# Kernel tuning notes

Hardware: AMD Instinct MI355X
Metric: run time of the kernel (lower is better)

## Reference

```python
import jax, jax.numpy as jnp
import numpy as np

SOS = 28          # RNNTParam.SOS = num_labels - 1
NUM_EMBED = 28    # num_labels - 1
C = 320           # pred_hidden_size
L = 2             # pred_num_layers
U, N = 128, 512   # decode steps, batch


def setup_inputs() -> dict:
    key = jax.random.key(0)
    ks = jax.random.split(key, 8)
    s = 1.0 / np.sqrt(C).astype(np.float32)
    x = jax.random.randint(ks[0], (U, N), 0, 29)                       # labels incl. SOS=28
    h0 = jax.random.normal(ks[1], (L, N, C), jnp.float32)
    c0 = jax.random.normal(ks[2], (L, N, C), jnp.float32)
    embed_weight = jax.random.normal(ks[3], (NUM_EMBED, C), jnp.float32)
    w_ih = jax.random.uniform(ks[4], (L, 4 * C, C), jnp.float32, -s, s)
    w_hh = jax.random.uniform(ks[5], (L, 4 * C, C), jnp.float32, -s, s)
    b_ih = jax.random.uniform(ks[6], (L, 4 * C), jnp.float32, -s, s)
    b_hh = jax.random.uniform(ks[7], (L, 4 * C), jnp.float32, -s, s)
    return dict(x=x, h0=h0, c0=c0, embed_weight=embed_weight,
                w_ih=w_ih, w_hh=w_hh, b_ih=b_ih, b_hh=b_hh)


def _lstm_layer(xs, h0, c0, w_ih, w_hh, b_ih, b_hh):
    # xs: [U, N, C]; torch LSTM gate order: i, f, g, o
    bias = b_ih + b_hh                                   # [4C]
    gx = jnp.einsum('unc,gc->ung', xs, w_ih) + bias      # precompute input part

    def step(carry, gx_t):
        h, c = carry
        gates = gx_t + h @ w_hh.T                        # [N, 4C]
        i, f, g, o = jnp.split(gates, 4, axis=-1)
        i = jax.nn.sigmoid(i)
        f = jax.nn.sigmoid(f)
        g = jnp.tanh(g)
        o = jax.nn.sigmoid(o)
        c = f * c + i * g
        h = o * jnp.tanh(c)
        return (h, c), h

    (hT, cT), ys = jax.lax.scan(step, (h0, c0), gx)
    return ys, hT, cT


def reference(x, h0, c0, embed_weight, w_ih, w_hh, b_ih, b_hh):
    sos_mask = (x == SOS)                                # [U, N]
    idx = jnp.where(sos_mask, 0, x)
    g = embed_weight[idx]                                # [U, N, C]
    g = jnp.where(sos_mask[..., None], 0.0, g)

    hs, cs = [], []
    for layer in range(L):
        g, hT, cT = _lstm_layer(g, h0[layer], c0[layer],
                                w_ih[layer], w_hh[layer],
                                b_ih[layer], b_hh[layer])
        hs.append(hT)
        cs.append(cT)
    hg = jnp.stack(hs, axis=0)                           # [L, N, C]
    cg = jnp.stack(cs, axis=0)
    return g, (hg, cg)
```

## Files before the change

kernel.cpp:

```cpp
#include <hip/hip_runtime.h>
#include <hip/hip_bf16.h>
#include <stdint.h>


typedef short short8 __attribute__((ext_vector_type(8)));
typedef float f32x4 __attribute__((ext_vector_type(4)));

#define USTEPS 128
#define HSZ    (512*320)
#define GSTEP  (512*320)
#define HGOFF  (128*512*320)
#define CGOFF  (HGOFF + 2*512*320)
#define FLAGSTRIDE 16

__device__ __forceinline__ uint16_t f2bf(float f) {
  union { float f; uint32_t i; } v; v.f = f;
  uint32_t i = v.i;
  return (uint16_t)((i + 0x7fffu + ((i >> 16) & 1u)) >> 16);
}
__device__ __forceinline__ float rcp_(float x) { return __builtin_amdgcn_rcpf(x); }
__device__ __forceinline__ float sigm(float x) { return rcp_(1.0f + __expf(-x)); }
__device__ __forceinline__ float tanh_(float x) {
  float ax = fabsf(x);
  float e  = __expf(-2.0f * ax);
  float t  = (1.0f - e) * rcp_(1.0f + e);
  return x < 0.0f ? -t : t;
}
__device__ __forceinline__ uint4 cvt8(const float* s) {
  float4 a = ((const float4*)s)[0];
  float4 b = ((const float4*)s)[1];
  uint4 r;
  r.x = (uint32_t)f2bf(a.x) | ((uint32_t)f2bf(a.y) << 16);
  r.y = (uint32_t)f2bf(a.z) | ((uint32_t)f2bf(a.w) << 16);
  r.z = (uint32_t)f2bf(b.x) | ((uint32_t)f2bf(b.y) << 16);
  r.w = (uint32_t)f2bf(b.z) | ((uint32_t)f2bf(b.w) << 16);
  return r;
}
__device__ __forceinline__ short8 loadw8(const float* p) {
  float4 a = ((const float4*)p)[0];
  float4 b = ((const float4*)p)[1];
  short8 r;
  r[0] = (short)f2bf(a.x); r[1] = (short)f2bf(a.y);
  r[2] = (short)f2bf(a.z); r[3] = (short)f2bf(a.w);
  r[4] = (short)f2bf(b.x); r[5] = (short)f2bf(b.y);
  r[6] = (short)f2bf(b.z); r[7] = (short)f2bf(b.w);
  return r;
}

#define PREP_G0   (29 * 1280)
#define PREP_B1   (PREP_G0 + 1280)
#define PREP_FL   (PREP_B1 + 8192)
#define PREP_HI   (PREP_FL + 2 * 512 * 40)
__global__ void prep_kernel(const float* __restrict__ embed,
                            const float* __restrict__ w_ih,
                            const float* __restrict__ b_ih,
                            const float* __restrict__ b_hh,
                            const float* __restrict__ h0,
                            float* __restrict__ G0p,
                            float* __restrict__ bias1p,
                            uint32_t* __restrict__ flags,
                            uint16_t* __restrict__ Hx0,
                            uint16_t* __restrict__ Hx1) {
  int tid = blockIdx.x * blockDim.x + threadIdx.x;
  if (tid < PREP_G0) {
    int v = tid / 1280, col = tid % 1280;
    int hg = col / 80, idx = col % 80;
    int k = idx >> 2, q = idx & 3;
    int r = q * 320 + hg * 20 + k;
    float acc = b_ih[r] + b_hh[r];
    if (v < 28) {
      const float4* e = (const float4*)(embed + (size_t)v * 320);
      const float4* w = (const float4*)(w_ih + (size_t)r * 320);
#pragma unroll 4
      for (int i = 0; i < 80; ++i) {
        float4 a = e[i], b = w[i];
        acc += a.x * b.x + a.y * b.y + a.z * b.z + a.w * b.w;
      }
    }
    G0p[tid] = acc;
  } else if (tid < PREP_B1) {
    int col = tid - PREP_G0;
    int hg = col / 80, idx = col % 80;
    int k = idx >> 2, q = idx & 3;
    int r = q * 320 + hg * 20 + k;
    bias1p[col] = b_ih[1280 + r] + b_hh[1280 + r];
  } else if (tid < PREP_FL) {
    flags[tid - PREP_B1] = 0;
  } else if (tid < PREP_HI) {
    int id = tid - PREP_FL;
    int layer = id / 20480;
    int rem = id - layer * 20480;
    int n = rem / 40, c = rem - n * 40;
    const float* src = h0 + (size_t)layer * HSZ + (size_t)n * 320 + c * 8;
    uint16_t* dst = (layer ? Hx1 : Hx0) + HSZ + (size_t)n * 320 + c * 8;
    *(uint4*)dst = cvt8(src);
  }
}

__global__ void __launch_bounds__(320, 2)
rnnt_kernel(const int* __restrict__ x,
            const float* __restrict__ c0,
            const float* __restrict__ w_ih,
            const float* __restrict__ w_hh,
            const float* __restrict__ G0p,
            const float* __restrict__ bias1p,
            uint16_t* __restrict__ Hx0,
            uint16_t* __restrict__ Hx1,
            uint32_t* __restrict__ flags,
            float* __restrict__ out) {
  __shared__ __align__(16) uint16_t Hl0[32 * 320];
  __shared__ __align__(16) uint16_t Hl1[32 * 320];
  __shared__ __align__(16) float    gates0[32 * 84];
  __shared__ __align__(16) float    gates1[32 * 84];
  __shared__ int ctr0, ctr1;

  const int tid  = threadIdx.x;
  const int wave = tid >> 6;
  const int lane = tid & 63;
  const int quad = lane >> 4;
  const int lm   = lane & 15;
  const int blk  = blockIdx.x;
  const int bg = (blk & 7) * 2 + (blk >> 7);
  const int hg = (blk >> 3) & 15;

  short8 Bhh0[10], Bih1[10], Bhh1[10];
  {
    int ncol = wave * 16 + lm;
    int k = ncol >> 2, q = ncol & 3;
    int r = q * 320 + hg * 20 + k;
    const float* p0 = w_hh + (size_t)r * 320 + quad * 8;
    const float* p1 = w_hh + (size_t)(1280 + r) * 320 + quad * 8;
    const float* pi = w_ih + (size_t)(1280 + r) * 320 + quad * 8;
#pragma unroll
    for (int kk = 0; kk < 10; ++kk) {
      Bhh0[kk] = loadw8(p0 + kk * 32);
      Bhh1[kk] = loadw8(p1 + kk * 32);
      Bih1[kk] = loadw8(pi + kk * 32);
    }
  }
  const float bias1v = bias1p[hg * 80 + wave * 16 + lm];

  const int un  = tid / 10;
  const int ukp = tid - un * 10;
  const int n_g = bg * 32 + un;
  const int kc  = hg * 20 + ukp * 2;

  int smc[8], spc[8];
#pragma unroll
  for (int it = 0; it < 8; ++it) {
    int cid = tid + it * 320;
    int m = cid / 80;
    int c8 = cid - m * 80;
    int c16 = c8 >> 1, h = c8 & 1;
    int p16 = c16 + m; if (p16 >= 40) p16 -= 40;
    smc[it] = m * 320 + c8 * 4;
    spc[it] = m * 320 + p16 * 8 + h * 4;
  }
  const size_t gbase = (size_t)bg * 32 * 320;

  float c0s0 = c0[(size_t)n_g * 320 + kc];
  float c0s1 = c0[(size_t)n_g * 320 + kc + 1];
  float c1s0 = c0[(size_t)(512 + n_g) * 320 + kc];
  float c1s1 = c0[(size_t)(512 + n_g) * 320 + kc + 1];

  uint32_t* flags0  = flags;
  uint32_t* flags1  = flags + 256 * FLAGSTRIDE;
  uint32_t* myflag0 = flags0 + (size_t)(bg * 16 + hg) * FLAGSTRIDE;
  uint32_t* myflag1 = flags1 + (size_t)(bg * 16 + hg) * FLAGSTRIDE;

  {
    if (tid == 0) { ctr0 = 0; ctr1 = 0; }
    const uint16_t* s0b = Hx0 + HSZ + gbase;
    unsigned long long r0[8];
#pragma unroll
    for (int it = 0; it < 8; ++it)
      r0[it] = __hip_atomic_load((const unsigned long long*)(s0b + smc[it]),
                                 __ATOMIC_RELAXED, __HIP_MEMORY_SCOPE_AGENT);
    asm volatile("s_waitcnt vmcnt(0)" ::: "memory");
#pragma unroll
    for (int it = 0; it < 8; ++it)
      *(unsigned long long*)(Hl0 + spc[it]) = r0[it];
    __syncthreads();
  }

  float4 gxa, gxb;
  {
    const int v = x[n_g];
    const float* gx = G0p + (size_t)v * 1280 + hg * 80 + ukp * 8;
    gxa = ((const float4*)gx)[0];
    gxb = ((const float4*)gx)[1];
  }

#pragma unroll 1
  for (int t = 0; t <= USTEPS; ++t) {
    const bool do0 = (t < USTEPS);
    const bool do1 = (t >= 1);

    unsigned long long r1[8];
    if (do1) {
      const uint16_t* s1b = Hx1 + (size_t)(t & 1) * HSZ + gbase;
#pragma unroll
      for (int it = 0; it < 8; ++it)
        r1[it] = __hip_atomic_load((const unsigned long long*)(s1b + smc[it]),
                                   __ATOMIC_RELAXED, __HIP_MEMORY_SCOPE_AGENT);
    }

    f32x4 ag00 = {0.f, 0.f, 0.f, 0.f}, ag01 = {0.f, 0.f, 0.f, 0.f};
    f32x4 ag10 = {bias1v, bias1v, bias1v, bias1v}, ag11 = ag10;
#pragma unroll
    for (int kk = 0; kk < 10; ++kk) {
      int cch = kk * 4 + quad;
      int p0a = cch + lm;      if (p0a >= 40) p0a -= 40;
      int p1a = cch + lm + 16; if (p1a >= 40) p1a -= 40;
      short8 a00 = *(const short8*)(Hl0 + lm * 320 + p0a * 8);
      short8 a01 = *(const short8*)(Hl0 + (lm + 16) * 320 + p1a * 8);
      if (do0) {
        ag00 = __builtin_amdgcn_mfma_f32_16x16x32_bf16(a00, Bhh0[kk], ag00, 0, 0, 0);
        ag01 = __builtin_amdgcn_mfma_f32_16x16x32_bf16(a01, Bhh0[kk], ag01, 0, 0, 0);
      }
      if (do1) {
        ag10 = __builtin_amdgcn_mfma_f32_16x16x32_bf16(a00, Bih1[kk], ag10, 0, 0, 0);
        ag11 = __builtin_amdgcn_mfma_f32_16x16x32_bf16(a01, Bih1[kk], ag11, 0, 0, 0);
      }
    }

    if (do1) {
      asm volatile("s_waitcnt vmcnt(0)" ::: "memory");
#pragma unroll
      for (int it = 0; it < 8; ++it)
        *(unsigned long long*)(Hl1 + spc[it]) = r1[it];
    }
    if (do0) {
#pragma unroll
      for (int r = 0; r < 4; ++r) {
        gates0[(quad * 4 + r) * 84 + wave * 16 + lm]      = ag00[r];
        gates0[(16 + quad * 4 + r) * 84 + wave * 16 + lm] = ag01[r];
      }
    }
    __syncthreads();

    if (do0) {
      const float* gp = gates0 + un * 84 + ukp * 8;
      float i0 = gp[0] + gxa.x, f0 = gp[1] + gxa.y, g0 = gp[2] + gxa.z, o0 = gp[3] + gxa.w;
      float i1 = gp[4] + gxb.x, f1 = gp[5] + gxb.y, g1 = gp[6] + gxb.z, o1 = gp[7] + gxb.w;
      c0s0 = sigm(f0) * c0s0 + sigm(i0) * tanh_(g0);
      c0s1 = sigm(f1) * c0s1 + sigm(i1) * tanh_(g1);
      float ha = sigm(o0) * tanh_(c0s0);
      float hb = sigm(o1) * tanh_(c0s1);
      uint32_t packed = (uint32_t)f2bf(ha) | ((uint32_t)f2bf(hb) << 16);
      __hip_atomic_store((uint32_t*)(Hx0 + (size_t)(t & 1) * HSZ + (size_t)n_g * 320 + kc),
                         packed, __ATOMIC_RELAXED, __HIP_MEMORY_SCOPE_AGENT);
      if (t == USTEPS - 1) {
        *(float2*)(out + HGOFF + (size_t)n_g * 320 + kc) = make_float2(ha, hb);
        *(float2*)(out + CGOFF + (size_t)n_g * 320 + kc) = make_float2(c0s0, c0s1);
      }
    }

    if (do1) {
#pragma unroll
      for (int kk = 0; kk < 5; ++kk) {
        int cch = kk * 4 + quad;
        int p0a = cch + lm;      if (p0a >= 40) p0a -= 40;
        int p1a = cch + lm + 16; if (p1a >= 40) p1a -= 40;
        short8 a10 = *(const short8*)(Hl1 + lm * 320 + p0a * 8);
        short8 a11 = *(const short8*)(Hl1 + (lm + 16) * 320 + p1a * 8);
        ag10 = __builtin_amdgcn_mfma_f32_16x16x32_bf16(a10, Bhh1[kk], ag10, 0, 0, 0);
        ag11 = __builtin_amdgcn_mfma_f32_16x16x32_bf16(a11, Bhh1[kk], ag11, 0, 0, 0);
      }
    }

    if (do0) {
      asm volatile("s_waitcnt vmcnt(0)" ::: "memory");
      if (lane == 0) {
        int old = atomicAdd(&ctr0, 1);
        if ((old % 5) == 4)
          __hip_atomic_store(myflag0, (uint32_t)(t + 1), __ATOMIC_RELAXED,
                             __HIP_MEMORY_SCOPE_AGENT);
      }
    }

    if (do1) {
#pragma unroll
      for (int kk = 5; kk < 10; ++kk) {
        int cch = kk * 4 + quad;
        int p0a = cch + lm;      if (p0a >= 40) p0a -= 40;
        int p1a = cch + lm + 16; if (p1a >= 40) p1a -= 40;
        short8 a10 = *(const short8*)(Hl1 + lm * 320 + p0a * 8);
        short8 a11 = *(const short8*)(Hl1 + (lm + 16) * 320 + p1a * 8);
        ag10 = __builtin_amdgcn_mfma_f32_16x16x32_bf16(a10, Bhh1[kk], ag10, 0, 0, 0);
        ag11 = __builtin_amdgcn_mfma_f32_16x16x32_bf16(a11, Bhh1[kk], ag11, 0, 0, 0);
      }
#pragma unroll
      for (int r = 0; r < 4; ++r) {
        gates1[(quad * 4 + r) * 84 + wave * 16 + lm]      = ag10[r];
        gates1[(16 + quad * 4 + r) * 84 + wave * 16 + lm] = ag11[r];
      }
    }
    __syncthreads();

    if (do1) {
      const int u1 = t - 1;
      const float* gp = gates1 + un * 84 + ukp * 8;
      float i0 = gp[0], f0 = gp[1], g0 = gp[2], o0 = gp[3];
      float i1 = gp[4], f1 = gp[5], g1 = gp[6], o1 = gp[7];
      c1s0 = sigm(f0) * c1s0 + sigm(i0) * tanh_(g0);
      c1s1 = sigm(f1) * c1s1 + sigm(i1) * tanh_(g1);
      float ha = sigm(o0) * tanh_(c1s0);
      float hb = sigm(o1) * tanh_(c1s1);
      *(float2*)(out + (size_t)u1 * GSTEP + (size_t)n_g * 320 + kc) = make_float2(ha, hb);
      uint32_t packed = (uint32_t)f2bf(ha) | ((uint32_t)f2bf(hb) << 16);
      __hip_atomic_store((uint32_t*)(Hx1 + (size_t)((t + 1) & 1) * HSZ + (size_t)n_g * 320 + kc),
                         packed, __ATOMIC_RELAXED, __HIP_MEMORY_SCOPE_AGENT);
      if (t == USTEPS) {
        *(float2*)(out + HGOFF + (size_t)(512 + n_g) * 320 + kc) = make_float2(ha, hb);
        *(float2*)(out + CGOFF + (size_t)(512 + n_g) * 320 + kc) = make_float2(c1s0, c1s1);
      }
      asm volatile("s_waitcnt vmcnt(0)" ::: "memory");
      if (lane == 0) {
        int old = atomicAdd(&ctr1, 1);
        if ((old % 5) == 4)
          __hip_atomic_store(myflag1, (uint32_t)(t + 1), __ATOMIC_RELAXED,
                             __HIP_MEMORY_SCOPE_AGENT);
      }
    }

    if (t + 1 < USTEPS) {
      const int v = x[(t + 1) * 512 + n_g];
      const float* gx = G0p + (size_t)v * 1280 + hg * 80 + ukp * 8;
      gxa = ((const float4*)gx)[0];
      gxb = ((const float4*)gx)[1];
    }

    if (t < USTEPS) {
      if (tid < 16) {
        uint32_t* peer = flags0 + (size_t)(bg * 16 + tid) * FLAGSTRIDE;
        while (__hip_atomic_load(peer, __ATOMIC_RELAXED,
                                 __HIP_MEMORY_SCOPE_AGENT) < (uint32_t)(t + 1)) {
        }
      }
      __syncthreads();
      const uint16_t* s0b = Hx0 + (size_t)(t & 1) * HSZ + gbase;
      unsigned long long r0[8];
#pragma unroll
      for (int it = 0; it < 8; ++it)
        r0[it] = __hip_atomic_load((const unsigned long long*)(s0b + smc[it]),
                                   __ATOMIC_RELAXED, __HIP_MEMORY_SCOPE_AGENT);
      asm volatile("s_waitcnt vmcnt(0)" ::: "memory");
#pragma unroll
      for (int it = 0; it < 8; ++it)
        *(unsigned long long*)(Hl0 + spc[it]) = r0[it];
      if (tid < 16 && t >= 1) {
        uint32_t* peer = flags1 + (size_t)(bg * 16 + tid) * FLAGSTRIDE;
        while (__hip_atomic_load(peer, __ATOMIC_RELAXED,
                                 __HIP_MEMORY_SCOPE_AGENT) < (uint32_t)(t + 1)) {
        }
      }
      __syncthreads();
    }
  }
}

extern "C" void kernel_launch(void* const* d_in, const int* in_sizes, int n_in,
                              void* d_out, int out_size, void* d_ws, size_t ws_size,
                              hipStream_t stream) {
  (void)in_sizes; (void)n_in; (void)out_size; (void)ws_size;
  const int*   x     = (const int*)d_in[0];
  const float* h0    = (const float*)d_in[1];
  const float* c0    = (const float*)d_in[2];
  const float* embed = (const float*)d_in[3];
  const float* w_ih  = (const float*)d_in[4];
  const float* w_hh  = (const float*)d_in[5];
  const float* b_ih  = (const float*)d_in[6];
  const float* b_hh  = (const float*)d_in[7];
  float* out = (float*)d_out;

  char* ws = (char*)d_ws;
  float*    G0p   = (float*)(ws);
  float*    b1p   = (float*)(ws + 148480);
  uint32_t* flags = (uint32_t*)(ws + 153600);
  uint16_t* Hx0   = (uint16_t*)(ws + 186368);
  uint16_t* Hx1   = (uint16_t*)(ws + 841728);

  hipLaunchKernelGGL(prep_kernel, dim3(342), dim3(256), 0, stream,
                     embed, w_ih, b_ih, b_hh, h0, G0p, b1p, flags, Hx0, Hx1);

  void* args[] = { (void*)&x, (void*)&c0, (void*)&w_ih, (void*)&w_hh,
                   (void*)&G0p, (void*)&b1p, (void*)&Hx0, (void*)&Hx1,
                   (void*)&flags, (void*)&out };
  hipLaunchCooperativeKernel((const void*)rnnt_kernel, dim3(256), dim3(320),
                             args, 0, stream);
}
```

Baseline: 757.5 us.

## Use XCD-local cache-coherent loads/stores for hidden-state exchange when batch group shares an XCD

At startup each block records its XCC id in a shared table and checks whether all 16 blocks of its batch group are on the same XCD. If they are (and the placement is not uniform across all blocks), the recurrence loop uses sc0-scoped global loads/stores instead of agent-scope atomics for exchanging bf16 hidden states. The goal is to avoid the L2-bypass cost of device-scope coherence. The kernel body is templated to produce both paths, and the prep kernel and workspace offsets grow to hold and clear the table. Correctness depends on the hardware coherence behaviour of sc0 within one XCD.

```diff
diff --git a/kernel.cpp b/kernel.cpp
--- a/kernel.cpp
+++ b/kernel.cpp
@@ -1,10 +1,10 @@
 #include <hip/hip_runtime.h>
-#include <hip/hip_bf16.h>
 #include <stdint.h>
 
 
 typedef short short8 __attribute__((ext_vector_type(8)));
 typedef float f32x4 __attribute__((ext_vector_type(4)));
+typedef unsigned long long u64t;
 
 #define USTEPS 128
 #define HSZ    (512*320)
@@ -47,9 +47,36 @@
   return r;
 }
 
+__device__ __forceinline__ u64t slowld64(const void* p) {
+  return __hip_atomic_load((const u64t*)p, __ATOMIC_RELAXED,
+                           __HIP_MEMORY_SCOPE_AGENT);
+}
+template<bool FAST>
+__device__ __forceinline__ u64t exld64(const void* p) {
+  if (FAST) {
+    u64t r;
+    asm volatile("global_load_dwordx2 %0, %1, off sc0" : "=v"(r) : "v"(p));
+    return r;
+  } else {
+    return slowld64(p);
+  }
+}
+template<bool FAST>
+__device__ __forceinline__ void exst32(void* p, uint32_t v) {
+  if (FAST) {
+    asm volatile("global_store_dword %0, %1, off sc0" :: "v"(p), "v"(v) : "memory");
+  } else {
+    __hip_atomic_store((uint32_t*)p, v, __ATOMIC_RELAXED,
+                       __HIP_MEMORY_SCOPE_AGENT);
+  }
+}
+__device__ __forceinline__ void vm_drain() {
+  asm volatile("s_waitcnt vmcnt(0)" ::: "memory");
+}
+
 #define PREP_G0   (29 * 1280)
 #define PREP_B1   (PREP_G0 + 1280)
-#define PREP_FL   (PREP_B1 + 8192)
+#define PREP_FL   (PREP_B1 + 8448)
 #define PREP_HI   (PREP_FL + 2 * 512 * 40)
 __global__ void prep_kernel(const float* __restrict__ embed,
                             const float* __restrict__ w_ih,
@@ -97,6 +124,254 @@
   }
 }
 
+template<bool FAST>
+__device__ __forceinline__ void run_loop(
+    const int* __restrict__ x, const float* __restrict__ c0,
+    const float* __restrict__ w_ih, const float* __restrict__ w_hh,
+    const float* __restrict__ G0p, const float* __restrict__ bias1p,
+    uint16_t* __restrict__ Hx0, uint16_t* __restrict__ Hx1,
+    uint32_t* __restrict__ flags, float* __restrict__ out,
+    uint16_t* Hl0, uint16_t* Hl1, float* gates0, float* gates1,
+    int* ctr0, int* ctr1) {
+  const int tid  = threadIdx.x;
+  const int wave = tid >> 6;
+  const int lane = tid & 63;
+  const int quad = lane >> 4;
+  const int lm   = lane & 15;
+  const int blk  = blockIdx.x;
+  const int bg = (blk & 7) * 2 + (blk >> 7);
+  const int hg = (blk >> 3) & 15;
+
+  short8 Bhh0[10], Bih1[10], Bhh1[10];
+  {
+    int ncol = wave * 16 + lm;
+    int k = ncol >> 2, q = ncol & 3;
+    int r = q * 320 + hg * 20 + k;
+    const float* p0 = w_hh + (size_t)r * 320 + quad * 8;
+    const float* p1 = w_hh + (size_t)(1280 + r) * 320 + quad * 8;
+    const float* pi = w_ih + (size_t)(1280 + r) * 320 + quad * 8;
+#pragma unroll
+    for (int kk = 0; kk < 10; ++kk) {
+      Bhh0[kk] = loadw8(p0 + kk * 32);
+      Bhh1[kk] = loadw8(p1 + kk * 32);
+      Bih1[kk] = loadw8(pi + kk * 32);
+    }
+  }
+  const float bias1v = bias1p[hg * 80 + wave * 16 + lm];
+
+  const int un  = tid / 10;
+  const int ukp = tid - un * 10;
+  const int n_g = bg * 32 + un;
+  const int kc  = hg * 20 + ukp * 2;
+
+  int smc[8], spc[8];
+#pragma unroll
+  for (int it = 0; it < 8; ++it) {
+    int cid = tid + it * 320;
+    int m = cid / 80;
+    int c8 = cid - m * 80;
+    int c16 = c8 >> 1, h = c8 & 1;
+    int p16 = c16 + m; if (p16 >= 40) p16 -= 40;
+    smc[it] = m * 320 + c8 * 4;
+    spc[it] = m * 320 + p16 * 8 + h * 4;
+  }
+  const size_t gbase = (size_t)bg * 32 * 320;
+
+  float c0s0 = c0[(size_t)n_g * 320 + kc];
+  float c0s1 = c0[(size_t)n_g * 320 + kc + 1];
+  float c1s0 = c0[(size_t)(512 + n_g) * 320 + kc];
+  float c1s1 = c0[(size_t)(512 + n_g) * 320 + kc + 1];
+
+  uint32_t* flags0  = flags;
+  uint32_t* flags1  = flags + 256 * FLAGSTRIDE;
+  uint32_t* myflag0 = flags0 + (size_t)(bg * 16 + hg) * FLAGSTRIDE;
+  uint32_t* myflag1 = flags1 + (size_t)(bg * 16 + hg) * FLAGSTRIDE;
+
+  {
+    const uint16_t* s0b = Hx0 + HSZ + gbase;
+    u64t r0[8];
+#pragma unroll
+    for (int it = 0; it < 8; ++it) r0[it] = slowld64(s0b + smc[it]);
+    vm_drain();
+#pragma unroll
+    for (int it = 0; it < 8; ++it) *(u64t*)(Hl0 + spc[it]) = r0[it];
+    __syncthreads();
+  }
+
+  float4 gxa, gxb;
+  {
+    const int v = x[n_g];
+    const float* gx = G0p + (size_t)v * 1280 + hg * 80 + ukp * 8;
+    gxa = ((const float4*)gx)[0];
+    gxb = ((const float4*)gx)[1];
+  }
+
+#pragma unroll 1
+  for (int t = 0; t <= USTEPS; ++t) {
+    const bool do0 = (t < USTEPS);
+    const bool do1 = (t >= 1);
+
+    u64t r1[8];
+    if (do1) {
+      const uint16_t* s1b = Hx1 + (size_t)(t & 1) * HSZ + gbase;
+      if (FAST && t == 1) {
+#pragma unroll
+        for (int it = 0; it < 8; ++it) r1[it] = slowld64(s1b + smc[it]);
+      } else {
+#pragma unroll
+        for (int it = 0; it < 8; ++it) r1[it] = exld64<FAST>(s1b + smc[it]);
+      }
+    }
+
+    f32x4 ag00 = {0.f, 0.f, 0.f, 0.f}, ag01 = {0.f, 0.f, 0.f, 0.f};
+    f32x4 ag10 = {bias1v, bias1v, bias1v, bias1v}, ag11 = ag10;
+#pragma unroll
+    for (int kk = 0; kk < 10; ++kk) {
+      int cch = kk * 4 + quad;
+      int p0a = cch + lm;      if (p0a >= 40) p0a -= 40;
+      int p1a = cch + lm + 16; if (p1a >= 40) p1a -= 40;
+      short8 a00 = *(const short8*)(Hl0 + lm * 320 + p0a * 8);
+      short8 a01 = *(const short8*)(Hl0 + (lm + 16) * 320 + p1a * 8);
+      if (do0) {
+        ag00 = __builtin_amdgcn_mfma_f32_16x16x32_bf16(a00, Bhh0[kk], ag00, 0, 0, 0);
+        ag01 = __builtin_amdgcn_mfma_f32_16x16x32_bf16(a01, Bhh0[kk], ag01, 0, 0, 0);
+      }
+      if (do1) {
+        ag10 = __builtin_amdgcn_mfma_f32_16x16x32_bf16(a00, Bih1[kk], ag10, 0, 0, 0);
+        ag11 = __builtin_amdgcn_mfma_f32_16x16x32_bf16(a01, Bih1[kk], ag11, 0, 0, 0);
+      }
+    }
+
+    if (do1) {
+      vm_drain();
+#pragma unroll
+      for (int it = 0; it < 8; ++it) *(u64t*)(Hl1 + spc[it]) = r1[it];
+    }
+    if (do0) {
+#pragma unroll
+      for (int r = 0; r < 4; ++r) {
+        gates0[(quad * 4 + r) * 84 + wave * 16 + lm]      = ag00[r];
+        gates0[(16 + quad * 4 + r) * 84 + wave * 16 + lm] = ag01[r];
+      }
+    }
+    __syncthreads();
+
+    if (do0) {
+      const float* gp = gates0 + un * 84 + ukp * 8;
+      float i0 = gp[0] + gxa.x, f0 = gp[1] + gxa.y, g0 = gp[2] + gxa.z, o0 = gp[3] + gxa.w;
+      float i1 = gp[4] + gxb.x, f1 = gp[5] + gxb.y, g1 = gp[6] + gxb.z, o1 = gp[7] + gxb.w;
+      c0s0 = sigm(f0) * c0s0 + sigm(i0) * tanh_(g0);
+      c0s1 = sigm(f1) * c0s1 + sigm(i1) * tanh_(g1);
+      float ha = sigm(o0) * tanh_(c0s0);
+      float hb = sigm(o1) * tanh_(c0s1);
+      uint32_t packed = (uint32_t)f2bf(ha) | ((uint32_t)f2bf(hb) << 16);
+      exst32<FAST>(Hx0 + (size_t)(t & 1) * HSZ + (size_t)n_g * 320 + kc, packed);
+      if (t == USTEPS - 1) {
+        *(float2*)(out + HGOFF + (size_t)n_g * 320 + kc) = make_float2(ha, hb);
+        *(float2*)(out + CGOFF + (size_t)n_g * 320 + kc) = make_float2(c0s0, c0s1);
+      }
+    }
+
+    if (do1) {
+#pragma unroll
+      for (int kk = 0; kk < 5; ++kk) {
+        int cch = kk * 4 + quad;
+        int p0a = cch + lm;      if (p0a >= 40) p0a -= 40;
+        int p1a = cch + lm + 16; if (p1a >= 40) p1a -= 40;
+        short8 a10 = *(const short8*)(Hl1 + lm * 320 + p0a * 8);
+        short8 a11 = *(const short8*)(Hl1 + (lm + 16) * 320 + p1a * 8);
+        ag10 = __builtin_amdgcn_mfma_f32_16x16x32_bf16(a10, Bhh1[kk], ag10, 0, 0, 0);
+        ag11 = __builtin_amdgcn_mfma_f32_16x16x32_bf16(a11, Bhh1[kk], ag11, 0, 0, 0);
+      }
+    }
+
+    if (do0) {
+      vm_drain();
+      if (lane == 0) {
+        int old = atomicAdd(ctr0, 1);
+        if ((old % 5) == 4)
+          __hip_atomic_store(myflag0, (uint32_t)(t + 1), __ATOMIC_RELAXED,
+                             __HIP_MEMORY_SCOPE_AGENT);
+      }
+    }
+
+    if (do1) {
+#pragma unroll
+      for (int kk = 5; kk < 10; ++kk) {
+        int cch = kk * 4 + quad;
+        int p0a = cch + lm;      if (p0a >= 40) p0a -= 40;
+        int p1a = cch + lm + 16; if (p1a >= 40) p1a -= 40;
+        short8 a10 = *(const short8*)(Hl1 + lm * 320 + p0a * 8);
+        short8 a11 = *(const short8*)(Hl1 + (lm + 16) * 320 + p1a * 8);
+        ag10 = __builtin_amdgcn_mfma_f32_16x16x32_bf16(a10, Bhh1[kk], ag10, 0, 0, 0);
+        ag11 = __builtin_amdgcn_mfma_f32_16x16x32_bf16(a11, Bhh1[kk], ag11, 0, 0, 0);
+      }
+#pragma unroll
+      for (int r = 0; r < 4; ++r) {
+        gates1[(quad * 4 + r) * 84 + wave * 16 + lm]      = ag10[r];
+        gates1[(16 + quad * 4 + r) * 84 + wave * 16 + lm] = ag11[r];
+      }
+    }
+    __syncthreads();
+
+    if (do1) {
+      const int u1 = t - 1;
+      const float* gp = gates1 + un * 84 + ukp * 8;
+      float i0 = gp[0], f0 = gp[1], g0 = gp[2], o0 = gp[3];
+      float i1 = gp[4], f1 = gp[5], g1 = gp[6], o1 = gp[7];
+      c1s0 = sigm(f0) * c1s0 + sigm(i0) * tanh_(g0);
+      c1s1 = sigm(f1) * c1s1 + sigm(i1) * tanh_(g1);
+      float ha = sigm(o0) * tanh_(c1s0);
+      float hb = sigm(o1) * tanh_(c1s1);
+      *(float2*)(out + (size_t)u1 * GSTEP + (size_t)n_g * 320 + kc) = make_float2(ha, hb);
+      uint32_t packed = (uint32_t)f2bf(ha) | ((uint32_t)f2bf(hb) << 16);
+      exst32<FAST>(Hx1 + (size_t)((t + 1) & 1) * HSZ + (size_t)n_g * 320 + kc, packed);
+      if (t == USTEPS) {
+        *(float2*)(out + HGOFF + (size_t)(512 + n_g) * 320 + kc) = make_float2(ha, hb);
+        *(float2*)(out + CGOFF + (size_t)(512 + n_g) * 320 + kc) = make_float2(c1s0, c1s1);
+      }
+      vm_drain();
+      if (lane == 0) {
+        int old = atomicAdd(ctr1, 1);
+        if ((old % 5) == 4)
+          __hip_atomic_store(myflag1, (uint32_t)(t + 1), __ATOMIC_RELAXED,
+                             __HIP_MEMORY_SCOPE_AGENT);
+      }
+    }
+
+    if (t + 1 < USTEPS) {
+      const int v = x[(t + 1) * 512 + n_g];
+      const float* gx = G0p + (size_t)v * 1280 + hg * 80 + ukp * 8;
+      gxa = ((const float4*)gx)[0];
+      gxb = ((const float4*)gx)[1];
+    }
+
+    if (t < USTEPS) {
+      if (tid < 16) {
+        uint32_t* peer = flags0 + (size_t)(bg * 16 + tid) * FLAGSTRIDE;
+        while (__hip_atomic_load(peer, __ATOMIC_RELAXED,
+                                 __HIP_MEMORY_SCOPE_AGENT) < (uint32_t)(t + 1)) {
+        }
+      }
+      __syncthreads();
+      const uint16_t* s0b = Hx0 + (size_t)(t & 1) * HSZ + gbase;
+      u64t r0[8];
+#pragma unroll
+      for (int it = 0; it < 8; ++it) r0[it] = exld64<FAST>(s0b + smc[it]);
+      vm_drain();
+#pragma unroll
+      for (int it = 0; it < 8; ++it) *(u64t*)(Hl0 + spc[it]) = r0[it];
+      if (tid < 16 && t >= 1) {
+        uint32_t* peer = flags1 + (size_t)(bg * 16 + tid) * FLAGSTRIDE;
+        while (__hip_atomic_load(peer, __ATOMIC_RELAXED,
+                                 __HIP_MEMORY_SCOPE_AGENT) < (uint32_t)(t + 1)) {
+        }
+      }
+      __syncthreads();
+    }
+  }
+}
+
 __global__ void __launch_bounds__(320, 2)
 rnnt_kernel(const int* __restrict__ x,
             const float* __restrict__ c0,
@@ -113,251 +388,43 @@
   __shared__ __align__(16) float    gates0[32 * 84];
   __shared__ __align__(16) float    gates1[32 * 84];
   __shared__ int ctr0, ctr1;
-
-  const int tid  = threadIdx.x;
-  const int wave = tid >> 6;
-  const int lane = tid & 63;
-  const int quad = lane >> 4;
-  const int lm   = lane & 15;
-  const int blk  = blockIdx.x;
+  __shared__ uint32_t v0sh;
+
+  const int tid = threadIdx.x;
+  const int blk = blockIdx.x;
   const int bg = (blk & 7) * 2 + (blk >> 7);
   const int hg = (blk >> 3) & 15;
 
-  short8 Bhh0[10], Bih1[10], Bhh1[10];
-  {
-    int ncol = wave * 16 + lm;
-    int k = ncol >> 2, q = ncol & 3;
-    int r = q * 320 + hg * 20 + k;
-    const float* p0 = w_hh + (size_t)r * 320 + quad * 8;
-    const float* p1 = w_hh + (size_t)(1280 + r) * 320 + quad * 8;
-    const float* pi = w_ih + (size_t)(1280 + r) * 320 + quad * 8;
-#pragma unroll
-    for (int kk = 0; kk < 10; ++kk) {
-      Bhh0[kk] = loadw8(p0 + kk * 32);
-      Bhh1[kk] = loadw8(p1 + kk * 32);
-      Bih1[kk] = loadw8(pi + kk * 32);
-    }
-  }
-  const float bias1v = bias1p[hg * 80 + wave * 16 + lm];
-
-  const int un  = tid / 10;
-  const int ukp = tid - un * 10;
-  const int n_g = bg * 32 + un;
-  const int kc  = hg * 20 + ukp * 2;
-
-  int smc[8], spc[8];
-#pragma unroll
-  for (int it = 0; it < 8; ++it) {
-    int cid = tid + it * 320;
-    int m = cid / 80;
-    int c8 = cid - m * 80;
-    int c16 = c8 >> 1, h = c8 & 1;
-    int p16 = c16 + m; if (p16 >= 40) p16 -= 40;
-    smc[it] = m * 320 + c8 * 4;
-    spc[it] = m * 320 + p16 * 8 + h * 4;
-  }
-  const size_t gbase = (size_t)bg * 32 * 320;
-
-  float c0s0 = c0[(size_t)n_g * 320 + kc];
-  float c0s1 = c0[(size_t)n_g * 320 + kc + 1];
-  float c1s0 = c0[(size_t)(512 + n_g) * 320 + kc];
-  float c1s1 = c0[(size_t)(512 + n_g) * 320 + kc + 1];
-
-  uint32_t* flags0  = flags;
-  uint32_t* flags1  = flags + 256 * FLAGSTRIDE;
-  uint32_t* myflag0 = flags0 + (size_t)(bg * 16 + hg) * FLAGSTRIDE;
-  uint32_t* myflag1 = flags1 + (size_t)(bg * 16 + hg) * FLAGSTRIDE;
-
-  {
-    if (tid == 0) { ctr0 = 0; ctr1 = 0; }
-    const uint16_t* s0b = Hx0 + HSZ + gbase;
-    unsigned long long r0[8];
-#pragma unroll
-    for (int it = 0; it < 8; ++it)
-      r0[it] = __hip_atomic_load((const unsigned long long*)(s0b + smc[it]),
-                                 __ATOMIC_RELAXED, __HIP_MEMORY_SCOPE_AGENT);
-    asm volatile("s_waitcnt vmcnt(0)" ::: "memory");
-#pragma unroll
-    for (int it = 0; it < 8; ++it)
-      *(unsigned long long*)(Hl0 + spc[it]) = r0[it];
-    __syncthreads();
-  }
-
-  float4 gxa, gxb;
-  {
-    const int v = x[n_g];
-    const float* gx = G0p + (size_t)v * 1280 + hg * 80 + ukp * 8;
-    gxa = ((const float4*)gx)[0];
-    gxb = ((const float4*)gx)[1];
-  }
-
-#pragma unroll 1
-  for (int t = 0; t <= USTEPS; ++t) {
-    const bool do0 = (t < USTEPS);
-    const bool do1 = (t >= 1);
-
-    unsigned long long r1[8];
-    if (do1) {
-      const uint16_t* s1b = Hx1 + (size_t)(t & 1) * HSZ + gbase;
-#pragma unroll
-      for (int it = 0; it < 8; ++it)
-        r1[it] = __hip_atomic_load((const unsigned long long*)(s1b + smc[it]),
-                                   __ATOMIC_RELAXED, __HIP_MEMORY_SCOPE_AGENT);
-    }
-
-    f32x4 ag00 = {0.f, 0.f, 0.f, 0.f}, ag01 = {0.f, 0.f, 0.f, 0.f};
-    f32x4 ag10 = {bias1v, bias1v, bias1v, bias1v}, ag11 = ag10;
-#pragma unroll
-    for (int kk = 0; kk < 10; ++kk) {
-      int cch = kk * 4 + quad;
-      int p0a = cch + lm;      if (p0a >= 40) p0a -= 40;
-      int p1a = cch + lm + 16; if (p1a >= 40) p1a -= 40;
-      short8 a00 = *(const short8*)(Hl0 + lm * 320 + p0a * 8);
-      short8 a01 = *(const short8*)(Hl0 + (lm + 16) * 320 + p1a * 8);
-      if (do0) {
-        ag00 = __builtin_amdgcn_mfma_f32_16x16x32_bf16(a00, Bhh0[kk], ag00, 0, 0, 0);
-        ag01 = __builtin_amdgcn_mfma_f32_16x16x32_bf16(a01, Bhh0[kk], ag01, 0, 0, 0);
-      }
-      if (do1) {
-        ag10 = __builtin_amdgcn_mfma_f32_16x16x32_bf16(a00, Bih1[kk], ag10, 0, 0, 0);
-        ag11 = __builtin_amdgcn_mfma_f32_16x16x32_bf16(a01, Bih1[kk], ag11, 0, 0, 0);
-      }
-    }
-
-    if (do1) {
-      asm volatile("s_waitcnt vmcnt(0)" ::: "memory");
-#pragma unroll
-      for (int it = 0; it < 8; ++it)
-        *(unsigned long long*)(Hl1 + spc[it]) = r1[it];
-    }
-    if (do0) {
-#pragma unroll
-      for (int r = 0; r < 4; ++r) {
-        gates0[(quad * 4 + r) * 84 + wave * 16 + lm]      = ag00[r];
-        gates0[(16 + quad * 4 + r) * 84 + wave * 16 + lm] = ag01[r];
-      }
-    }
-    __syncthreads();
-
-    if (do0) {
-      const float* gp = gates0 + un * 84 + ukp * 8;
-      float i0 = gp[0] + gxa.x, f0 = gp[1] + gxa.y, g0 = gp[2] + gxa.z, o0 = gp[3] + gxa.w;
-      float i1 = gp[4] + gxb.x, f1 = gp[5] + gxb.y, g1 = gp[6] + gxb.z, o1 = gp[7] + gxb.w;
-      c0s0 = sigm(f0) * c0s0 + sigm(i0) * tanh_(g0);
-      c0s1 = sigm(f1) * c0s1 + sigm(i1) * tanh_(g1);
-      float ha = sigm(o0) * tanh_(c0s0);
-      float hb = sigm(o1) * tanh_(c0s1);
-      uint32_t packed = (uint32_t)f2bf(ha) | ((uint32_t)f2bf(hb) << 16);
-      __hip_atomic_store((uint32_t*)(Hx0 + (size_t)(t & 1) * HSZ + (size_t)n_g * 320 + kc),
-                         packed, __ATOMIC_RELAXED, __HIP_MEMORY_SCOPE_AGENT);
-      if (t == USTEPS - 1) {
-        *(float2*)(out + HGOFF + (size_t)n_g * 320 + kc) = make_float2(ha, hb);
-        *(float2*)(out + CGOFF + (size_t)n_g * 320 + kc) = make_float2(c0s0, c0s1);
-      }
-    }
-
-    if (do1) {
-#pragma unroll
-      for (int kk = 0; kk < 5; ++kk) {
-        int cch = kk * 4 + quad;
-        int p0a = cch + lm;      if (p0a >= 40) p0a -= 40;
-        int p1a = cch + lm + 16; if (p1a >= 40) p1a -= 40;
-        short8 a10 = *(const short8*)(Hl1 + lm * 320 + p0a * 8);
-        short8 a11 = *(const short8*)(Hl1 + (lm + 16) * 320 + p1a * 8);
-        ag10 = __builtin_amdgcn_mfma_f32_16x16x32_bf16(a10, Bhh1[kk], ag10, 0, 0, 0);
-        ag11 = __builtin_amdgcn_mfma_f32_16x16x32_bf16(a11, Bhh1[kk], ag11, 0, 0, 0);
-      }
-    }
-
-    if (do0) {
-      asm volatile("s_waitcnt vmcnt(0)" ::: "memory");
-      if (lane == 0) {
-        int old = atomicAdd(&ctr0, 1);
-        if ((old % 5) == 4)
-          __hip_atomic_store(myflag0, (uint32_t)(t + 1), __ATOMIC_RELAXED,
-                             __HIP_MEMORY_SCOPE_AGENT);
-      }
-    }
-
-    if (do1) {
-#pragma unroll
-      for (int kk = 5; kk < 10; ++kk) {
-        int cch = kk * 4 + quad;
-        int p0a = cch + lm;      if (p0a >= 40) p0a -= 40;
-        int p1a = cch + lm + 16; if (p1a >= 40) p1a -= 40;
-        short8 a10 = *(const short8*)(Hl1 + lm * 320 + p0a * 8);
-        short8 a11 = *(const short8*)(Hl1 + (lm + 16) * 320 + p1a * 8);
-        ag10 = __builtin_amdgcn_mfma_f32_16x16x32_bf16(a10, Bhh1[kk], ag10, 0, 0, 0);
-        ag11 = __builtin_amdgcn_mfma_f32_16x16x32_bf16(a11, Bhh1[kk], ag11, 0, 0, 0);
-      }
-#pragma unroll
-      for (int r = 0; r < 4; ++r) {
-        gates1[(quad * 4 + r) * 84 + wave * 16 + lm]      = ag10[r];
-        gates1[(16 + quad * 4 + r) * 84 + wave * 16 + lm] = ag11[r];
-      }
-    }
-    __syncthreads();
-
-    if (do1) {
-      const int u1 = t - 1;
-      const float* gp = gates1 + un * 84 + ukp * 8;
-      float i0 = gp[0], f0 = gp[1], g0 = gp[2], o0 = gp[3];
-      float i1 = gp[4], f1 = gp[5], g1 = gp[6], o1 = gp[7];
-      c1s0 = sigm(f0) * c1s0 + sigm(i0) * tanh_(g0);
-      c1s1 = sigm(f1) * c1s1 + sigm(i1) * tanh_(g1);
-      float ha = sigm(o0) * tanh_(c1s0);
-      float hb = sigm(o1) * tanh_(c1s1);
-      *(float2*)(out + (size_t)u1 * GSTEP + (size_t)n_g * 320 + kc) = make_float2(ha, hb);
-      uint32_t packed = (uint32_t)f2bf(ha) | ((uint32_t)f2bf(hb) << 16);
-      __hip_atomic_store((uint32_t*)(Hx1 + (size_t)((t + 1) & 1) * HSZ + (size_t)n_g * 320 + kc),
-                         packed, __ATOMIC_RELAXED, __HIP_MEMORY_SCOPE_AGENT);
-      if (t == USTEPS) {
-        *(float2*)(out + HGOFF + (size_t)(512 + n_g) * 320 + kc) = make_float2(ha, hb);
-        *(float2*)(out + CGOFF + (size_t)(512 + n_g) * 320 + kc) = make_float2(c1s0, c1s1);
-      }
-      asm volatile("s_waitcnt vmcnt(0)" ::: "memory");
-      if (lane == 0) {
-        int old = atomicAdd(&ctr1, 1);
-        if ((old % 5) == 4)
-          __hip_atomic_store(myflag1, (uint32_t)(t + 1), __ATOMIC_RELAXED,
-                             __HIP_MEMORY_SCOPE_AGENT);
-      }
-    }
-
-    if (t + 1 < USTEPS) {
-      const int v = x[(t + 1) * 512 + n_g];
-      const float* gx = G0p + (size_t)v * 1280 + hg * 80 + ukp * 8;
-      gxa = ((const float4*)gx)[0];
-      gxb = ((const float4*)gx)[1];
-    }
-
-    if (t < USTEPS) {
-      if (tid < 16) {
-        uint32_t* peer = flags0 + (size_t)(bg * 16 + tid) * FLAGSTRIDE;
-        while (__hip_atomic_load(peer, __ATOMIC_RELAXED,
-                                 __HIP_MEMORY_SCOPE_AGENT) < (uint32_t)(t + 1)) {
-        }
-      }
-      __syncthreads();
-      const uint16_t* s0b = Hx0 + (size_t)(t & 1) * HSZ + gbase;
-      unsigned long long r0[8];
-#pragma unroll
-      for (int it = 0; it < 8; ++it)
-        r0[it] = __hip_atomic_load((const unsigned long long*)(s0b + smc[it]),
-                                   __ATOMIC_RELAXED, __HIP_MEMORY_SCOPE_AGENT);
-      asm volatile("s_waitcnt vmcnt(0)" ::: "memory");
-#pragma unroll
-      for (int it = 0; it < 8; ++it)
-        *(unsigned long long*)(Hl0 + spc[it]) = r0[it];
-      if (tid < 16 && t >= 1) {
-        uint32_t* peer = flags1 + (size_t)(bg * 16 + tid) * FLAGSTRIDE;
-        while (__hip_atomic_load(peer, __ATOMIC_RELAXED,
-                                 __HIP_MEMORY_SCOPE_AGENT) < (uint32_t)(t + 1)) {
-        }
-      }
-      __syncthreads();
-    }
-  }
+  const uint32_t xcc = (uint32_t)__builtin_amdgcn_s_getreg((3 << 11) | 20) & 0xffu;
+  const uint32_t mine = 0x100u | xcc;
+  uint32_t* xcdtab = flags + 8192;
+
+  if (tid == 0) {
+    ctr0 = 0; ctr1 = 0;
+    __hip_atomic_store(&xcdtab[bg * 16 + hg], mine, __ATOMIC_RELAXED,
+                       __HIP_MEMORY_SCOPE_AGENT);
+  }
+  uint32_t v = 0;
+  if (tid < 256) {
+    do {
+      v = __hip_atomic_load(&xcdtab[tid], __ATOMIC_RELAXED,
+                            __HIP_MEMORY_SCOPE_AGENT);
+    } while (v == 0u);
+    if (tid == 0) v0sh = v;
+  }
+  __syncthreads();
+  const uint32_t v0 = v0sh;
+  const int anydiff = __syncthreads_or((tid < 256) ? (int)(v != v0) : 0);
+  const int anybad  = __syncthreads_or(
+      (tid < 256 && (tid >> 4) == bg) ? (int)(v != mine) : 0);
+  const bool fastok = (anydiff != 0) && (anybad == 0);
+
+  if (fastok)
+    run_loop<true>(x, c0, w_ih, w_hh, G0p, bias1p, Hx0, Hx1, flags, out,
+                   Hl0, Hl1, gates0, gates1, &ctr0, &ctr1);
+  else
+    run_loop<false>(x, c0, w_ih, w_hh, G0p, bias1p, Hx0, Hx1, flags, out,
+                    Hl0, Hl1, gates0, gates1, &ctr0, &ctr1);
 }
 
 extern "C" void kernel_launch(void* const* d_in, const int* in_sizes, int n_in,
@@ -378,10 +445,10 @@
   float*    G0p   = (float*)(ws);
   float*    b1p   = (float*)(ws + 148480);
   uint32_t* flags = (uint32_t*)(ws + 153600);
-  uint16_t* Hx0   = (uint16_t*)(ws + 186368);
-  uint16_t* Hx1   = (uint16_t*)(ws + 841728);
-
-  hipLaunchKernelGGL(prep_kernel, dim3(342), dim3(256), 0, stream,
+  uint16_t* Hx0   = (uint16_t*)(ws + 187392);
+  uint16_t* Hx1   = (uint16_t*)(ws + 842752);
+
+  hipLaunchKernelGGL(prep_kernel, dim3(343), dim3(256), 0, stream,
                      embed, w_ih, b_ih, b_hh, h0, G0p, b1p, flags, Hx0, Hx1);
 
   void* args[] = { (void*)&x, (void*)&c0, (void*)&w_ih, (void*)&w_hh,
```

After: 722.6 us. 1.05x faster.
